# Optimization experiments

Measured on AMD Instinct MI355X. Metric: run time of the kernel, lower is better.

## Reference

```python
import jax, jax.numpy as jnp
import numpy as np

WS = 8      # window size
S = 2       # num_heads
GRID = jnp.linspace(-2.0, 2.0, 8)  # RBF grid, num_grids=8
DENOM = 4.0 / 7.0                  # (grid_max-grid_min)/(num_grids-1)


def _layernorm(x, g, b, eps=1e-5):
    mu = x.mean(-1, keepdims=True)
    var = ((x - mu) ** 2).mean(-1, keepdims=True)
    return (x - mu) * jax.lax.rsqrt(var + eps) * g + b


def _fastkan(x, ln_g, ln_b, ws, wb, bb):
    # x: (..., in_dim). RBF basis: (..., in_dim, 8) -> flatten -> spline GEMM; plus SiLU base path.
    ln = _layernorm(x, ln_g, ln_b)
    basis = jnp.exp(-(((ln[..., None] - GRID) / DENOM) ** 2))
    flat = basis.reshape(*basis.shape[:-2], -1)
    return flat @ ws.T + jax.nn.silu(x) @ wb.T + bb


def setup_inputs() -> dict:
    key = jax.random.key(0)
    ks = jax.random.split(key, 16)
    d = {
        'x': jax.random.normal(ks[0], (4, 32, 256, 256), dtype=jnp.float32),
        'pn_g': jnp.ones((32,), jnp.float32), 'pn_b': jnp.zeros((32,), jnp.float32),
        'k1_ln_g': jnp.ones((16,), jnp.float32), 'k1_ln_b': jnp.zeros((16,), jnp.float32),
        'k1_ws': jax.random.normal(ks[1], (16, 128), jnp.float32) * 0.1,
        'k1_wb': jax.random.normal(ks[2], (16, 16), jnp.float32) * 0.1,
        'k1_bb': jnp.zeros((16,), jnp.float32),
        'k2_ln_g': jnp.ones((16,), jnp.float32), 'k2_ln_b': jnp.zeros((16,), jnp.float32),
        'k2_ws': jax.random.normal(ks[3], (16, 128), jnp.float32) * 0.1,
        'k2_wb': jax.random.normal(ks[4], (16, 16), jnp.float32) * 0.1,
        'k2_bb': jnp.zeros((16,), jnp.float32),
        'k3_ln_g': jnp.ones((32,), jnp.float32), 'k3_ln_b': jnp.zeros((32,), jnp.float32),
        'k3_ws': jax.random.normal(ks[5], (32, 256), jnp.float32) * 0.1,
        'k3_wb': jax.random.normal(ks[6], (32, 32), jnp.float32) * 0.1,
        'k3_bb': jnp.zeros((32,), jnp.float32),
        'k4_ln_g': jnp.ones((32,), jnp.float32), 'k4_ln_b': jnp.zeros((32,), jnp.float32),
        'k4_ws': jax.random.normal(ks[7], (32, 256), jnp.float32) * 0.1,
        'k4_wb': jax.random.normal(ks[8], (32, 32), jnp.float32) * 0.1,
        'k4_bb': jnp.zeros((32,), jnp.float32),
    }
    return d


def reference(x, pn_g, pn_b,
              k1_ln_g, k1_ln_b, k1_ws, k1_wb, k1_bb,
              k2_ln_g, k2_ln_b, k2_ws, k2_wb, k2_bb,
              k3_ln_g, k3_ln_b, k3_ws, k3_wb, k3_bb,
              k4_ln_g, k4_ln_b, k4_ws, k4_wb, k4_bb):
    B, C, H, W = x.shape
    c = C // S
    # b c h w -> b h w c, then window partition (shift_size=0, no padding)
    xh = jnp.transpose(x, (0, 2, 3, 1))
    wins = xh.reshape(B, H // WS, WS, W // WS, WS, C).transpose(0, 1, 3, 2, 4, 5).reshape(-1, WS, WS, C)
    b = wins.shape[0]
    # PreNormResidual
    y = _layernorm(wins, pn_g, pn_b)
    # branch 1: 'b h w (c s) -> b (w c) (h s)'
    a = y.reshape(b, WS, WS, c, S).transpose(0, 2, 3, 1, 4).reshape(b, WS * c, WS * S)
    a = _fastkan(a, k1_ln_g, k1_ln_b, k1_ws, k1_wb, k1_bb)
    a = a.reshape(b, WS, c, WS, S).transpose(0, 3, 1, 2, 4).reshape(b, WS, WS, C)
    # branch 2: 'b h w (c s) -> b (h c) (w s)'
    d = y.reshape(b, WS, WS, c, S).transpose(0, 1, 3, 2, 4).reshape(b, WS * c, WS * S)
    d = _fastkan(d, k2_ln_g, k2_ln_b, k2_ws, k2_wb, k2_bb)
    d = d.reshape(b, WS, c, WS, S).transpose(0, 1, 3, 2, 4).reshape(b, WS, WS, C)
    # branch 3: channel mixing
    e = _fastkan(y.reshape(b, WS * WS, C), k3_ln_g, k3_ln_b, k3_ws, k3_wb, k3_bb).reshape(b, WS, WS, C)
    z = a + d + e
    # output KAN layer then residual
    z = _fastkan(z.reshape(b, WS * WS, C), k4_ln_g, k4_ln_b, k4_ws, k4_wb, k4_bb).reshape(b, WS, WS, C)
    out = z + wins
    # window reverse, back to b c h w
    out = out.reshape(B, H // WS, W // WS, WS, WS, C).transpose(0, 1, 3, 2, 4, 5).reshape(B, H, W, C)
    return jnp.transpose(out, (0, 3, 1, 2))
```

## Files before the change

### kernel.cpp

```cpp
#include <hip/hip_runtime.h>

typedef __attribute__((ext_vector_type(8))) short  s8v;
typedef __attribute__((ext_vector_type(8))) __bf16 b8v;
typedef __attribute__((ext_vector_type(2))) __bf16 b2v;
typedef __attribute__((ext_vector_type(4))) float  f4v;
typedef __attribute__((ext_vector_type(2))) float  f2v;

#define LDST 36
#define SWST 40

#define W2_OFF 2560
#define W3_OFF 5120
#define W4_OFF 14336
#define W_TOTAL 23552
#define PREP_TOTAL (192 + W_TOTAL)

__device__ __forceinline__ float frcp_(float x){ return __builtin_amdgcn_rcpf(x); }
__device__ __forceinline__ float rsq_(float x){ return __builtin_amdgcn_rsqf(x); }
__device__ __forceinline__ float silu_(float x){ return x * frcp_(1.0f + __expf(-x)); }

__device__ __forceinline__ s8v b2s(b8v v){ union { b8v b; s8v s; } u; u.b = v; return u.s; }

__device__ __forceinline__ b8v basis8bf_(float u){
  float b = __expf(-u*u);
  float A = __expf(2.0f*u);
  b8v r;
  r[0] = (__bf16)b;
  b *= A * 0.36787944117144233f;   r[1] = (__bf16)b;
  b *= A * 0.049787068367863944f;  r[2] = (__bf16)b;
  b *= A * 0.006737946999085467f;  r[3] = (__bf16)b;
  b *= A * 0.0009118819655545162f; r[4] = (__bf16)b;
  b *= A * 1.2340980408667956e-4f; r[5] = (__bf16)b;
  b *= A * 1.670170079024566e-5f;  r[6] = (__bf16)b;
  b *= A * 2.2603294069810542e-6f; r[7] = (__bf16)b;
  return r;
}

__global__ void prep_w(const float* __restrict__ ws1, const float* __restrict__ wb1,
                       const float* __restrict__ ws2, const float* __restrict__ wb2,
                       const float* __restrict__ ws3, const float* __restrict__ wb3,
                       const float* __restrict__ ws4, const float* __restrict__ wb4,
                       const float* __restrict__ g1, const float* __restrict__ b1,
                       const float* __restrict__ g2, const float* __restrict__ b2,
                       const float* __restrict__ g3, const float* __restrict__ b3,
                       const float* __restrict__ g4, const float* __restrict__ b4,
                       float* __restrict__ LNP, __bf16* __restrict__ W){
  int idx = blockIdx.x*256 + threadIdx.x;
  if (idx >= PREP_TOTAL) return;
  if (idx < 192){
    float v;
    if      (idx < 16)  v = 1.75f * g1[idx];
    else if (idx < 32)  v = 1.75f * (b1[idx-16] + 2.0f);
    else if (idx < 48)  v = 1.75f * g2[idx-32];
    else if (idx < 64)  v = 1.75f * (b2[idx-48] + 2.0f);
    else if (idx < 96)  v = 1.75f * g3[idx-64];
    else if (idx < 128) v = 1.75f * (b3[idx-96] + 2.0f);
    else if (idx < 160) v = 1.75f * g4[idx-128];
    else                v = 1.75f * (b4[idx-160] + 2.0f);
    LNP[idx] = v;
    return;
  }
  int widx = idx - 192;
  float v;
  if (widx < W3_OFF){
    int base = (widx >= W2_OFF) ? W2_OFF : 0;
    const float* ws = base ? ws2 : ws1;
    const float* wb = base ? wb2 : wb1;
    int r = widx - base; int o = r/160, k = r%160;
    if (k < 128){
      int ks = k>>5, kg = (k>>3)&3, j = k&7;
      int elem = kg*4 + ks;
      v = ws[o*128 + elem*8 + j];
    } else {
      int kk = k-128; int kg = kk>>3, j = kk&7;
      v = (j<4) ? wb[o*16 + kg*4 + j] : 0.0f;
    }
  } else {
    int base = (widx >= W4_OFF) ? W4_OFF : W3_OFF;
    const float* ws = (base == W4_OFF) ? ws4 : ws3;
    const float* wb = (base == W4_OFF) ? wb4 : wb3;
    int r = widx - base; int o = r/288, k = r%288;
    if (k < 256){
      int ks = k>>5, kg = (k>>3)&3, j = k&7;
      int elem = kg*8 + ks;
      v = ws[o*256 + elem*8 + j];
    } else {
      int kk = k-256; int kg = kk>>3, j = kk&7;
      v = wb[o*32 + kg*8 + j];
    }
  }
  W[widx] = (__bf16)v;
}

__global__ __launch_bounds__(256,4)
void swin_kan_mfma(const float* __restrict__ x,
                   const float* __restrict__ pn_g, const float* __restrict__ pn_b,
                   const float* __restrict__ k1_bb, const float* __restrict__ k2_bb,
                   const float* __restrict__ k3_bb, const float* __restrict__ k4_bb,
                   const float* __restrict__ LNP,
                   const __bf16* __restrict__ Wbf,
                   float* __restrict__ out)
{
  __shared__ __attribute__((aligned(16))) float  yw[64][LDST];
  __shared__ __attribute__((aligned(16))) float  zA[64][LDST];
  __shared__ __attribute__((aligned(16))) __bf16 sw[64][SWST];
  __shared__ __attribute__((aligned(16))) float  LNPs[192];

  const int t   = threadIdx.x;
  const int bid = blockIdx.x;
  const int wid = (bid & 7)*512 + (bid >> 3);
  const int b   = wid >> 10;
  const int h0  = ((wid >> 5) & 31) * 8;
  const int w0  = (wid & 31) * 8;
  const int wave = t >> 6;
  const int lane = t & 63;
  const int fn = lane & 15, kg = lane >> 4;

  {
    int ch = t & 31, h = t >> 5;
    const float* src = x + (((size_t)(b*32 + ch)*256 + (h0+h))*256 + w0);
    float4 v0 = *(const float4*)(src);
    float4 v1 = *(const float4*)(src + 4);
    int p = h*8;
    yw[p+0][ch]=v0.x; yw[p+1][ch]=v0.y; yw[p+2][ch]=v0.z; yw[p+3][ch]=v0.w;
    yw[p+4][ch]=v1.x; yw[p+5][ch]=v1.y; yw[p+6][ch]=v1.z; yw[p+7][ch]=v1.w;
    if (t < 192) LNPs[t] = LNP[t];
  }
  __syncthreads();

  {
    int pos = t >> 2, part = t & 3;
    f4v a = *(const f4v*)&yw[pos][part*8];
    f4v c = *(const f4v*)&yw[pos][part*8+4];
    float s1 = a[0]+a[1]+a[2]+a[3]+c[0]+c[1]+c[2]+c[3];
    float s2 = a[0]*a[0]+a[1]*a[1]+a[2]*a[2]+a[3]*a[3]
             + c[0]*c[0]+c[1]*c[1]+c[2]*c[2]+c[3]*c[3];
    s1 += __shfl_xor(s1,1); s2 += __shfl_xor(s2,1);
    s1 += __shfl_xor(s1,2); s2 += __shfl_xor(s2,2);
    float mu  = s1*(1.0f/32.0f);
    float var = s2*(1.0f/32.0f) - mu*mu;
    float rs  = rsq_(var + 1e-5f);
    f4v g0 = *(const f4v*)&pn_g[part*8], g1 = *(const f4v*)&pn_g[part*8+4];
    f4v b0 = *(const f4v*)&pn_b[part*8], b1 = *(const f4v*)&pn_b[part*8+4];
    f4v o0, o1;
    #pragma unroll
    for (int j=0;j<4;j++){ o0[j] = (a[j]-mu)*rs*g0[j] + b0[j]; o1[j] = (c[j]-mu)*rs*g1[j] + b1[j]; }
    *(f4v*)&yw[pos][part*8]   = o0;
    *(f4v*)&yw[pos][part*8+4] = o1;
    b8v sl;
    #pragma unroll
    for (int j=0;j<4;j++){ sl[j] = (__bf16)silu_(o0[j]); sl[4+j] = (__bf16)silu_(o1[j]); }
    *(b8v*)&sw[pos][part*8] = sl;
  }
  __syncthreads();

  {
    const bool br2 = (wave >= 2);
    const __bf16* Wp  = Wbf + (br2 ? W2_OFF : 0);
    const float* bbp = br2 ? k2_bb : k1_bb;
    const int gb = br2 ? 32 : 0, b2b = gb + 16;
    s8v wfr[5];
    #pragma unroll
    for (int ks=0;ks<5;ks++) wfr[ks] = *(const s8v*)&Wp[fn*160 + ks*32 + kg*8];
    f4v bias = *(const f4v*)&bbp[kg*4];
    f4v G  = *(const f4v*)&LNPs[gb  + kg*4];
    f4v B2 = *(const f4v*)&LNPs[b2b + kg*4];

    f4v accs[4];
    #pragma unroll
    for (int mi=0; mi<4; mi++){
      const int ck = (wave & 1)*4 + mi;
      const int posA = br2 ? (ck*8 + 2*kg) : ((2*kg)*8 + ck);
      const int posB = posA + (br2 ? 1 : 8);
      f2v va = *(const f2v*)&yw[posA][2*fn];
      f2v vb = *(const f2v*)&yw[posB][2*fn];
      b2v sa = *(const b2v*)&sw[posA][2*fn];
      b2v sb = *(const b2v*)&sw[posB][2*fn];
      float v[4] = { va[0], va[1], vb[0], vb[1] };
      b8v bb = {};
      bb[0]=sa[0]; bb[1]=sa[1]; bb[2]=sb[0]; bb[3]=sb[1];

      float s1 = v[0]+v[1]+v[2]+v[3];
      float s2 = v[0]*v[0]+v[1]*v[1]+v[2]*v[2]+v[3]*v[3];
      s1 += __shfl_xor(s1,16); s2 += __shfl_xor(s2,16);
      s1 += __shfl_xor(s1,32); s2 += __shfl_xor(s2,32);
      float mu  = s1*(1.0f/16.0f);
      float var = s2*(1.0f/16.0f) - mu*mu;
      float rs  = rsq_(var + 1e-5f);

      f4v acc = bias;
      #pragma unroll
      for (int ks=0;ks<4;ks++){
        float pp = G[ks]*rs;
        float qq = __builtin_fmaf(-mu, pp, B2[ks]);
        float u  = __builtin_fmaf(v[ks], pp, qq);
        acc = __builtin_amdgcn_mfma_f32_16x16x32_bf16(wfr[ks], b2s(basis8bf_(u)), acc, 0,0,0);
      }
      acc = __builtin_amdgcn_mfma_f32_16x16x32_bf16(wfr[4], b2s(bb), acc, 0,0,0);
      accs[mi] = acc;
    }

    if (!br2){
      #pragma unroll
      for (int mi=0; mi<4; mi++){
        const int ck = (wave & 1)*4 + mi;
        *(f2v*)&zA[(2*kg+0)*8 + ck][2*fn] = f2v{accs[mi][0], accs[mi][1]};
        *(f2v*)&zA[(2*kg+1)*8 + ck][2*fn] = f2v{accs[mi][2], accs[mi][3]};
      }
    }
    __syncthreads();
    if (br2){
      #pragma unroll
      for (int mi=0; mi<4; mi++){
        const int ck = (wave & 1)*4 + mi;
        f2v o0 = *(f2v*)&zA[ck*8 + 2*kg+0][2*fn];
        f2v o1 = *(f2v*)&zA[ck*8 + 2*kg+1][2*fn];
        o0[0] += accs[mi][0]; o0[1] += accs[mi][1];
        o1[0] += accs[mi][2]; o1[1] += accs[mi][3];
        *(f2v*)&zA[ck*8 + 2*kg+0][2*fn] = o0;
        *(f2v*)&zA[ck*8 + 2*kg+1][2*fn] = o1;
      }
    }
  }
  __syncthreads();

  {
    const int r = wave*16 + fn;
    f4v v0 = *(const f4v*)&yw[r][kg*8];
    f4v v1 = *(const f4v*)&yw[r][kg*8+4];
    b8v bb = *(const b8v*)&sw[r][kg*8];
    float v[8] = { v0[0],v0[1],v0[2],v0[3], v1[0],v1[1],v1[2],v1[3] };
    float s1=0.f, s2=0.f;
    #pragma unroll
    for (int ks=0;ks<8;ks++){ s1 += v[ks]; s2 += v[ks]*v[ks]; }
    s1 += __shfl_xor(s1,16); s2 += __shfl_xor(s2,16);
    s1 += __shfl_xor(s1,32); s2 += __shfl_xor(s2,32);
    float mu  = s1*(1.0f/32.0f);
    float var = s2*(1.0f/32.0f) - mu*mu;
    float rs  = rsq_(var + 1e-5f);

    f4v Ga = *(const f4v*)&LNPs[64 + kg*8], Gb = *(const f4v*)&LNPs[64 + kg*8 + 4];
    f4v Ba = *(const f4v*)&LNPs[96 + kg*8], Bb = *(const f4v*)&LNPs[96 + kg*8 + 4];
    float G8[8]  = { Ga[0],Ga[1],Ga[2],Ga[3], Gb[0],Gb[1],Gb[2],Gb[3] };
    float B8[8]  = { Ba[0],Ba[1],Ba[2],Ba[3], Bb[0],Bb[1],Bb[2],Bb[3] };

    f4v acc0 = *(const f4v*)&k3_bb[kg*4];
    f4v acc1 = *(const f4v*)&k3_bb[16 + kg*4];
    #pragma unroll
    for (int ks=0;ks<8;ks++){
      float pp = G8[ks]*rs;
      float qq = __builtin_fmaf(-mu, pp, B8[ks]);
      float u  = __builtin_fmaf(v[ks], pp, qq);
      s8v bf = b2s(basis8bf_(u));
      s8v wa = *(const s8v*)&Wbf[W3_OFF + fn*288      + ks*32 + kg*8];
      s8v wb = *(const s8v*)&Wbf[W3_OFF + (16+fn)*288 + ks*32 + kg*8];
      acc0 = __builtin_amdgcn_mfma_f32_16x16x32_bf16(wa, bf, acc0, 0,0,0);
      acc1 = __builtin_amdgcn_mfma_f32_16x16x32_bf16(wb, bf, acc1, 0,0,0);
    }
    {
      s8v wa = *(const s8v*)&Wbf[W3_OFF + fn*288      + 256 + kg*8];
      s8v wb = *(const s8v*)&Wbf[W3_OFF + (16+fn)*288 + 256 + kg*8];
      acc0 = __builtin_amdgcn_mfma_f32_16x16x32_bf16(wa, b2s(bb), acc0, 0,0,0);
      acc1 = __builtin_amdgcn_mfma_f32_16x16x32_bf16(wb, b2s(bb), acc1, 0,0,0);
    }
    f4v za0 = *(const f4v*)&zA[r][kg*4];
    f4v za1 = *(const f4v*)&zA[r][16+kg*4];
    *(f4v*)&zA[r][kg*4]    = acc0 + za0;
    *(f4v*)&zA[r][16+kg*4] = acc1 + za1;
  }
  __syncthreads();

  {
    const int r = wave*16 + fn;
    f4v v0 = *(const f4v*)&zA[r][kg*8];
    f4v v1 = *(const f4v*)&zA[r][kg*8+4];
    float v[8] = { v0[0],v0[1],v0[2],v0[3], v1[0],v1[1],v1[2],v1[3] };
    float s1=0.f, s2=0.f;
    #pragma unroll
    for (int ks=0;ks<8;ks++){ s1 += v[ks]; s2 += v[ks]*v[ks]; }
    s1 += __shfl_xor(s1,16); s2 += __shfl_xor(s2,16);
    s1 += __shfl_xor(s1,32); s2 += __shfl_xor(s2,32);
    float mu  = s1*(1.0f/32.0f);
    float var = s2*(1.0f/32.0f) - mu*mu;
    float rs  = rsq_(var + 1e-5f);

    f4v Ga = *(const f4v*)&LNPs[128 + kg*8], Gb = *(const f4v*)&LNPs[128 + kg*8 + 4];
    f4v Ba = *(const f4v*)&LNPs[160 + kg*8], Bb = *(const f4v*)&LNPs[160 + kg*8 + 4];
    float G8[8]  = { Ga[0],Ga[1],Ga[2],Ga[3], Gb[0],Gb[1],Gb[2],Gb[3] };
    float B8[8]  = { Ba[0],Ba[1],Ba[2],Ba[3], Bb[0],Bb[1],Bb[2],Bb[3] };

    f4v acc0 = *(const f4v*)&k4_bb[kg*4];
    f4v acc1 = *(const f4v*)&k4_bb[16 + kg*4];
    b8v bb;
    #pragma unroll
    for (int ks=0;ks<8;ks++){
      float pp = G8[ks]*rs;
      float qq = __builtin_fmaf(-mu, pp, B8[ks]);
      float u  = __builtin_fmaf(v[ks], pp, qq);
      s8v bf = b2s(basis8bf_(u));
      s8v wa = *(const s8v*)&Wbf[W4_OFF + fn*288      + ks*32 + kg*8];
      s8v wb = *(const s8v*)&Wbf[W4_OFF + (16+fn)*288 + ks*32 + kg*8];
      acc0 = __builtin_amdgcn_mfma_f32_16x16x32_bf16(wa, bf, acc0, 0,0,0);
      acc1 = __builtin_amdgcn_mfma_f32_16x16x32_bf16(wb, bf, acc1, 0,0,0);
      bb[ks] = (__bf16)silu_(v[ks]);
    }
    {
      s8v wa = *(const s8v*)&Wbf[W4_OFF + fn*288      + 256 + kg*8];
      s8v wb = *(const s8v*)&Wbf[W4_OFF + (16+fn)*288 + 256 + kg*8];
      acc0 = __builtin_amdgcn_mfma_f32_16x16x32_bf16(wa, b2s(bb), acc0, 0,0,0);
      acc1 = __builtin_amdgcn_mfma_f32_16x16x32_bf16(wb, b2s(bb), acc1, 0,0,0);
    }
    *(f4v*)&yw[r][kg*4]    = acc0;
    *(f4v*)&yw[r][16+kg*4] = acc1;
  }
  __syncthreads();

  {
    int ch = t & 31, h = t >> 5;
    const size_t base = (((size_t)(b*32 + ch)*256 + (h0+h))*256 + w0);
    float4 xv0 = *(const float4*)(x + base);
    float4 xv1 = *(const float4*)(x + base + 4);
    int p = h*8;
    float4 v0 = { yw[p+0][ch]+xv0.x, yw[p+1][ch]+xv0.y, yw[p+2][ch]+xv0.z, yw[p+3][ch]+xv0.w };
    float4 v1 = { yw[p+4][ch]+xv1.x, yw[p+5][ch]+xv1.y, yw[p+6][ch]+xv1.z, yw[p+7][ch]+xv1.w };
    *(float4*)(out + base)     = v0;
    *(float4*)(out + base + 4) = v1;
  }
}

extern "C" void kernel_launch(void* const* d_in, const int* in_sizes, int n_in,
                              void* d_out, int out_size, void* d_ws, size_t ws_size,
                              hipStream_t stream) {
  const float* x      = (const float*)d_in[0];
  const float* pn_g   = (const float*)d_in[1];
  const float* pn_b   = (const float*)d_in[2];
  const float* k1_ln_g= (const float*)d_in[3];
  const float* k1_ln_b= (const float*)d_in[4];
  const float* k1_ws  = (const float*)d_in[5];
  const float* k1_wb  = (const float*)d_in[6];
  const float* k1_bb  = (const float*)d_in[7];
  const float* k2_ln_g= (const float*)d_in[8];
  const float* k2_ln_b= (const float*)d_in[9];
  const float* k2_ws  = (const float*)d_in[10];
  const float* k2_wb  = (const float*)d_in[11];
  const float* k2_bb  = (const float*)d_in[12];
  const float* k3_ln_g= (const float*)d_in[13];
  const float* k3_ln_b= (const float*)d_in[14];
  const float* k3_ws  = (const float*)d_in[15];
  const float* k3_wb  = (const float*)d_in[16];
  const float* k3_bb  = (const float*)d_in[17];
  const float* k4_ln_g= (const float*)d_in[18];
  const float* k4_ln_b= (const float*)d_in[19];
  const float* k4_ws  = (const float*)d_in[20];
  const float* k4_wb  = (const float*)d_in[21];
  const float* k4_bb  = (const float*)d_in[22];
  float* out = (float*)d_out;
  float*  LNP = (float*)d_ws;
  __bf16* Wbf = (__bf16*)((char*)d_ws + 768);

  hipLaunchKernelGGL(prep_w, dim3((PREP_TOTAL+255)/256), dim3(256), 0, stream,
                     k1_ws, k1_wb, k2_ws, k2_wb, k3_ws, k3_wb, k4_ws, k4_wb,
                     k1_ln_g, k1_ln_b, k2_ln_g, k2_ln_b,
                     k3_ln_g, k3_ln_b, k4_ln_g, k4_ln_b,
                     LNP, Wbf);

  hipLaunchKernelGGL(swin_kan_mfma, dim3(4096), dim3(256), 0, stream,
                     x, pn_g, pn_b,
                     k1_bb, k2_bb, k3_bb, k4_bb,
                     LNP, Wbf, out);
}
```

Baseline: 70.76 us.

## Replace block barriers with wave fences and drop SiLU LDS buffer

Three block-wide __syncthreads are replaced with wave-local LDS waitcnt fences. This is valid because each wave only reads the shared-memory rows it wrote itself in the load/LN, branch3→branch4 and branch4→store stages. The SiLU values are now recomputed from the normalized values in each consumer instead of being staged in a bf16 shared array, which removes one LDS buffer and its traffic at the cost of extra exp/rcp work. The input tile is also kept in registers for the final residual add instead of being reloaded from global memory, which adds register pressure.

```diff
diff --git a/kernel.cpp b/kernel.cpp
--- a/kernel.cpp
+++ b/kernel.cpp
@@ -7,7 +7,9 @@
 typedef __attribute__((ext_vector_type(2))) float  f2v;
 
 #define LDST 36
-#define SWST 40
+
+#define WAVE_FENCE() do { asm volatile("s_waitcnt lgkmcnt(0)" ::: "memory"); \
+                          __builtin_amdgcn_sched_barrier(0); } while(0)
 
 #define W2_OFF 2560
 #define W3_OFF 5120
@@ -103,7 +105,6 @@
 {
   __shared__ __attribute__((aligned(16))) float  yw[64][LDST];
   __shared__ __attribute__((aligned(16))) float  zA[64][LDST];
-  __shared__ __attribute__((aligned(16))) __bf16 sw[64][SWST];
   __shared__ __attribute__((aligned(16))) float  LNPs[192];
 
   const int t   = threadIdx.x;
@@ -116,17 +117,19 @@
   const int lane = t & 63;
   const int fn = lane & 15, kg = lane >> 4;
 
+  float4 xv0, xv1;
+
   {
     int ch = t & 31, h = t >> 5;
     const float* src = x + (((size_t)(b*32 + ch)*256 + (h0+h))*256 + w0);
-    float4 v0 = *(const float4*)(src);
-    float4 v1 = *(const float4*)(src + 4);
+    xv0 = *(const float4*)(src);
+    xv1 = *(const float4*)(src + 4);
     int p = h*8;
-    yw[p+0][ch]=v0.x; yw[p+1][ch]=v0.y; yw[p+2][ch]=v0.z; yw[p+3][ch]=v0.w;
-    yw[p+4][ch]=v1.x; yw[p+5][ch]=v1.y; yw[p+6][ch]=v1.z; yw[p+7][ch]=v1.w;
+    yw[p+0][ch]=xv0.x; yw[p+1][ch]=xv0.y; yw[p+2][ch]=xv0.z; yw[p+3][ch]=xv0.w;
+    yw[p+4][ch]=xv1.x; yw[p+5][ch]=xv1.y; yw[p+6][ch]=xv1.z; yw[p+7][ch]=xv1.w;
     if (t < 192) LNPs[t] = LNP[t];
   }
-  __syncthreads();
+  WAVE_FENCE();
 
   {
     int pos = t >> 2, part = t & 3;
@@ -147,10 +150,6 @@
     for (int j=0;j<4;j++){ o0[j] = (a[j]-mu)*rs*g0[j] + b0[j]; o1[j] = (c[j]-mu)*rs*g1[j] + b1[j]; }
     *(f4v*)&yw[pos][part*8]   = o0;
     *(f4v*)&yw[pos][part*8+4] = o1;
-    b8v sl;
-    #pragma unroll
-    for (int j=0;j<4;j++){ sl[j] = (__bf16)silu_(o0[j]); sl[4+j] = (__bf16)silu_(o1[j]); }
-    *(b8v*)&sw[pos][part*8] = sl;
   }
   __syncthreads();
 
@@ -174,11 +173,10 @@
       const int posB = posA + (br2 ? 1 : 8);
       f2v va = *(const f2v*)&yw[posA][2*fn];
       f2v vb = *(const f2v*)&yw[posB][2*fn];
-      b2v sa = *(const b2v*)&sw[posA][2*fn];
-      b2v sb = *(const b2v*)&sw[posB][2*fn];
       float v[4] = { va[0], va[1], vb[0], vb[1] };
       b8v bb = {};
-      bb[0]=sa[0]; bb[1]=sa[1]; bb[2]=sb[0]; bb[3]=sb[1];
+      #pragma unroll
+      for (int j=0;j<4;j++) bb[j] = (__bf16)silu_(v[j]);
 
       float s1 = v[0]+v[1]+v[2]+v[3];
       float s2 = v[0]*v[0]+v[1]*v[1]+v[2]*v[2]+v[3]*v[3];
@@ -228,8 +226,10 @@
     const int r = wave*16 + fn;
     f4v v0 = *(const f4v*)&yw[r][kg*8];
     f4v v1 = *(const f4v*)&yw[r][kg*8+4];
-    b8v bb = *(const b8v*)&sw[r][kg*8];
     float v[8] = { v0[0],v0[1],v0[2],v0[3], v1[0],v1[1],v1[2],v1[3] };
+    b8v bb;
+    #pragma unroll
+    for (int ks=0;ks<8;ks++) bb[ks] = (__bf16)silu_(v[ks]);
     float s1=0.f, s2=0.f;
     #pragma unroll
     for (int ks=0;ks<8;ks++){ s1 += v[ks]; s2 += v[ks]*v[ks]; }
@@ -268,7 +268,7 @@
     *(f4v*)&zA[r][kg*4]    = acc0 + za0;
     *(f4v*)&zA[r][16+kg*4] = acc1 + za1;
   }
-  __syncthreads();
+  WAVE_FENCE();
 
   {
     const int r = wave*16 + fn;
@@ -313,13 +313,11 @@
     *(f4v*)&yw[r][kg*4]    = acc0;
     *(f4v*)&yw[r][16+kg*4] = acc1;
   }
-  __syncthreads();
+  WAVE_FENCE();
 
   {
     int ch = t & 31, h = t >> 5;
     const size_t base = (((size_t)(b*32 + ch)*256 + (h0+h))*256 + w0);
-    float4 xv0 = *(const float4*)(x + base);
-    float4 xv1 = *(const float4*)(x + base + 4);
     int p = h*8;
     float4 v0 = { yw[p+0][ch]+xv0.x, yw[p+1][ch]+xv0.y, yw[p+2][ch]+xv0.z, yw[p+3][ch]+xv0.w };
     float4 v1 = { yw[p+4][ch]+xv1.x, yw[p+5][ch]+xv1.y, yw[p+6][ch]+xv1.z, yw[p+7][ch]+xv1.w };
```

New measurement: 67.65 us. -4.4%, faster.
